# Kernel tuning notes

Measured on AMD Instinct MI355X. Metric: run time of the kernel, lower is better.

## Reference

```python
import jax, jax.numpy as jnp
import numpy as np

B, LQ, LK = 16, 1024, 4096
QD, KD = 512, 512


def setup_inputs() -> dict:
    key = jax.random.key(0)
    ks = jax.random.split(key, 8)
    s = lambda d: 1.0 / np.sqrt(d)
    return {
        "query": jax.random.normal(ks[0], (B, LQ, QD), dtype=jnp.float32),
        "keys": jax.random.normal(ks[1], (B, LK, KD), dtype=jnp.float32),
        "Wq": jax.random.uniform(ks[2], (QD, KD), jnp.float32, -s(QD), s(QD)),
        "bq": jax.random.uniform(ks[3], (KD,), jnp.float32, -s(QD), s(QD)),
        "Wk": jax.random.uniform(ks[4], (KD, KD), jnp.float32, -s(KD), s(KD)),
        "bk": jax.random.uniform(ks[5], (KD,), jnp.float32, -s(KD), s(KD)),
        "Wv": jax.random.uniform(ks[6], (KD, KD), jnp.float32, -s(KD), s(KD)),
        "bv": jax.random.uniform(ks[7], (KD,), jnp.float32, -s(KD), s(KD)),
    }


def reference(query, keys, Wq, bq, Wk, bk, Wv, bv):
    scale = 1.0 / np.sqrt(KD)
    q = query @ Wq + bq                       # [B, LQ, KD]
    k = keys @ Wk + bk                        # [B, LK, KD]
    v = k @ Wv + bv                           # NOTE: value proj applied to projected keys (as in source)
    scores = jnp.einsum('bqd,bkd->bqk', q, k) * scale  # [B, LQ, LK]
    attn = jax.nn.softmax(scores, axis=2)
    context = jnp.einsum('bqk,bkd->bqd', attn, v)      # [B, LQ, KD]
    return context
```

## Files before the change

### kernel.cpp

```cpp
#include <hip/hip_runtime.h>
#include <hip/hip_bf16.h>
#include <stdint.h>


typedef __attribute__((ext_vector_type(8))) short bf16x8;
typedef __attribute__((ext_vector_type(4))) float f32x4;
typedef __attribute__((ext_vector_type(8))) unsigned short ushort8v;
typedef __attribute__((ext_vector_type(4))) unsigned short ushort4v;

__device__ __forceinline__ unsigned short f2bf(float f) {
  union { float f; unsigned int u; } x{f};
  unsigned int r = x.u + 0x7FFFu + ((x.u >> 16) & 1u);
  return (unsigned short)(r >> 16);
}
__device__ __forceinline__ float bf2f(unsigned short h) {
  union { unsigned int u; float f; } x{(unsigned int)h << 16};
  return x.f;
}

#define GLOAD_LDS16(gptr, lptr)                                                  \
  __builtin_amdgcn_global_load_lds((const __attribute__((address_space(1))) void*)(gptr), \
                                   (__attribute__((address_space(3))) void*)(lptr), 16, 0, 0)

__global__ __launch_bounds__(256) void cast_bf16_kernel(const float* __restrict__ in,
                                                        unsigned short* __restrict__ out,
                                                        long n) {
  long i = ((long)blockIdx.x * blockDim.x + threadIdx.x) * 8;
  long stride = (long)gridDim.x * blockDim.x * 8;
  for (; i < n; i += stride) {
    const float4* p = (const float4*)(in + i);
    float4 a = p[0], b = p[1];
    ushort8v o;
    o[0] = f2bf(a.x); o[1] = f2bf(a.y); o[2] = f2bf(a.z); o[3] = f2bf(a.w);
    o[4] = f2bf(b.x); o[5] = f2bf(b.y); o[6] = f2bf(b.z); o[7] = f2bf(b.w);
    *(ushort8v*)(out + i) = o;
  }
}

__global__ __launch_bounds__(256) void transpose_w_kernel(const float* __restrict__ W0,
                                                          const float* __restrict__ W1,
                                                          const float* __restrict__ W2,
                                                          unsigned short* __restrict__ T0,
                                                          unsigned short* __restrict__ T1,
                                                          unsigned short* __restrict__ T2) {
  const float* W = (blockIdx.z == 0) ? W0 : (blockIdx.z == 1) ? W1 : W2;
  unsigned short* T = (blockIdx.z == 0) ? T0 : (blockIdx.z == 1) ? T1 : T2;
  __shared__ float tile[32][33];
  int tx = threadIdx.x & 31, ty = threadIdx.x >> 5;
  int gx = blockIdx.x * 32 + tx;
  int gy0 = blockIdx.y * 32;
#pragma unroll
  for (int i = 0; i < 32; i += 8) tile[ty + i][tx] = W[(size_t)(gy0 + ty + i) * 512 + gx];
  __syncthreads();
  int ox = blockIdx.y * 32 + tx;
  int oy0 = blockIdx.x * 32;
#pragma unroll
  for (int i = 0; i < 32; i += 8)
    T[(size_t)(oy0 + ty + i) * 512 + ox] = f2bf(tile[tx][ty + i]);
}

template <int OUT_MODE>
__global__ __launch_bounds__(256, 2) void gemm_nt(const unsigned short* __restrict__ A,
                                                  const unsigned short* __restrict__ Bt,
                                                  const float* __restrict__ bias,
                                                  void* __restrict__ Cout,
                                                  int M, int N, int K, float scale) {
  __shared__ __align__(16) unsigned short lA[2][128][64];
  __shared__ __align__(16) unsigned short lB[2][128][64];
  const int tid = threadIdx.x;
  const int lane = tid & 63;
  const int wave = tid >> 6;
  const int m0 = blockIdx.y * 128;
  const int n0 = blockIdx.x * 128;

  f32x4 acc[4][4] = {};

  auto stage = [&](int buf, int kt) {
    const int k0 = kt * 64;
#pragma unroll
    for (int p = 0; p < 4; ++p) {
      int c = p * 4 + wave;
      int f = c * 512 + lane * 8;
      int row = f >> 6, col = f & 63;
      const unsigned short* gA = A + (size_t)(m0 + row) * K + (k0 + col);
      const unsigned short* gB = Bt + (size_t)(n0 + row) * K + (k0 + col);
      GLOAD_LDS16(gA, &lA[buf][0][0] + c * 512);
      GLOAD_LDS16(gB, &lB[buf][0][0] + c * 512);
    }
  };

  const int wm = wave >> 1, wn = wave & 1;
  const int lr = lane & 15;
  const int lk = (lane >> 4) << 3;

  const int KT = K >> 6;
  stage(0, 0);
  __syncthreads();
  int cur = 0;
  for (int kt = 0; kt < KT; ++kt) {
    if (kt + 1 < KT) stage(cur ^ 1, kt + 1);
#pragma unroll
    for (int kk = 0; kk < 64; kk += 32) {
      bf16x8 af[4], bfv[4];
#pragma unroll
      for (int i = 0; i < 4; ++i)
        af[i] = *(const bf16x8*)&lA[cur][wm * 64 + i * 16 + lr][kk + lk];
#pragma unroll
      for (int j = 0; j < 4; ++j)
        bfv[j] = *(const bf16x8*)&lB[cur][wn * 64 + j * 16 + lr][kk + lk];
#pragma unroll
      for (int i = 0; i < 4; ++i)
#pragma unroll
        for (int j = 0; j < 4; ++j)
          acc[i][j] = __builtin_amdgcn_mfma_f32_16x16x32_bf16(af[i], bfv[j], acc[i][j], 0, 0, 0);
    }
    __syncthreads();
    cur ^= 1;
  }

  const int ci = lane & 15;
  const int ri = (lane >> 4) * 4;
#pragma unroll
  for (int i = 0; i < 4; ++i) {
#pragma unroll
    for (int j = 0; j < 4; ++j) {
      int gm = m0 + wm * 64 + i * 16 + ri;
      int gn = n0 + wn * 64 + j * 16 + ci;
      float bv_ = bias[gn];
      f32x4 a = acc[i][j];
      if (OUT_MODE == 0) {
        unsigned short* C = (unsigned short*)Cout;
#pragma unroll
        for (int r = 0; r < 4; ++r)
          C[(size_t)(gm + r) * N + gn] = f2bf((a[r] + bv_) * scale);
      } else {
        unsigned short* C = (unsigned short*)Cout;
        int b_ = gm >> 12;
        int ml = gm & 4095;
        ushort4v pk;
#pragma unroll
        for (int r = 0; r < 4; ++r) pk[r] = f2bf((a[r] + bv_) * scale);
        *(ushort4v*)&C[((size_t)b_ * 512 + gn) * 4096 + ml] = pk;
      }
    }
  }
}

__global__ __launch_bounds__(512, 1) void flash_attn(const unsigned short* __restrict__ q,
                                                     const unsigned short* __restrict__ k,
                                                     const unsigned short* __restrict__ vT,
                                                     float* __restrict__ out) {
  __shared__ __align__(16) unsigned short lQ[64 * 512];
  __shared__ __align__(16) unsigned short lK[2][128 * 64];
  __shared__ __align__(16) unsigned short lP[64 * 128];
  __shared__ float redm[64 * 8], reds[64 * 8];
  __shared__ float m_s[64], rs_s[64];

  const int tid = threadIdx.x;
  const int lane = tid & 63;
  const int w = tid >> 6;
  const int bid = blockIdx.x;
  const int b = (bid & 7) * 2 + ((bid >> 3) >> 4);
  const int qt = (bid >> 3) & 15;

  const unsigned short* Qb = q + ((size_t)b * 1024 + qt * 64) * 512;
  const unsigned short* Kb = k + (size_t)b * 4096 * 512;
  const unsigned short* Vb = vT + (size_t)b * 512 * 4096;

  auto stageK = [&](int buf, int t2, int c2) {
    const int kv0 = t2 * 128, kk = c2 * 64;
#pragma unroll
    for (int i = 0; i < 2; ++i) {
      int byte = (i * 512 + tid) * 16;
      int row = byte >> 7;
      int colB = byte & 127;
      int srcB = colB ^ ((row & 7) << 4);
      GLOAD_LDS16(Kb + (size_t)(kv0 + row) * 512 + kk + (srcB >> 1),
                  (char*)&lK[buf][0] + byte);
    }
  };

#pragma unroll
  for (int i = 0; i < 8; ++i) {
    int byte = (i * 512 + tid) * 16;
    int row = byte >> 10;
    int colB = byte & 1023;
    int srcB = (colB & ~127) | ((colB & 127) ^ ((row & 7) << 4));
    GLOAD_LDS16(Qb + (size_t)row * 512 + (srcB >> 1), (char*)lQ + byte);
  }
  stageK(0, 0, 0);
  float m_run = -1e30f, l_run = 0.f;
  float rs_reg = 0.f;
  __syncthreads();

  f32x4 acc_o[4][4] = {};
  int cur = 0;

  for (int t = 0; t < 32; ++t) {
    f32x4 accS[4] = {};
    for (int c = 0; c < 8; ++c) {
      if (c < 7) stageK(cur ^ 1, t, c + 1);
      else if (t < 31) stageK(cur ^ 1, t + 1, 0);
      const int rowK = w * 16 + (lane & 15);
#pragma unroll
      for (int ks = 0; ks < 2; ++ks) {
        int colKB = ((ks * 64 + ((lane >> 4) << 4)) ^ ((rowK & 7) << 4));
        bf16x8 afK = *(const bf16x8*)((char*)&lK[cur][0] + rowK * 128 + colKB);
#pragma unroll
        for (int nf = 0; nf < 4; ++nf) {
          int rowQ = nf * 16 + (lane & 15);
          int colQB = c * 128 + ((ks * 64 + ((lane >> 4) << 4)) ^ ((rowQ & 7) << 4));
          bf16x8 bfQ = *(const bf16x8*)((char*)lQ + rowQ * 1024 + colQB);
          accS[nf] = __builtin_amdgcn_mfma_f32_16x16x32_bf16(afK, bfQ, accS[nf], 0, 0, 0);
        }
      }
      __syncthreads();
      cur ^= 1;
    }

#pragma unroll
    for (int nf = 0; nf < 4; ++nf) {
      f32x4 s = accS[nf];
      float mx = fmaxf(fmaxf(s[0], s[1]), fmaxf(s[2], s[3]));
      mx = fmaxf(mx, __shfl_xor(mx, 16));
      mx = fmaxf(mx, __shfl_xor(mx, 32));
      if (lane < 16) redm[(nf * 16 + lane) * 8 + w] = mx;
    }
    __syncthreads();
    if (w == 0) {
      f32x4 a = *(const f32x4*)&redm[lane * 8];
      f32x4 a2 = *(const f32x4*)&redm[lane * 8 + 4];
      float tmax = fmaxf(fmaxf(fmaxf(a[0], a[1]), fmaxf(a[2], a[3])),
                         fmaxf(fmaxf(a2[0], a2[1]), fmaxf(a2[2], a2[3])));
      float m_new = fmaxf(m_run, tmax);
      rs_reg = __expf(m_run - m_new);
      m_run = m_new;
      m_s[lane] = m_new;
      rs_s[lane] = rs_reg;
    }
    __syncthreads();
#pragma unroll
    for (int nf = 0; nf < 4; ++nf) {
      int qrow = nf * 16 + (lane & 15);
      float mq = m_s[qrow];
      f32x4 s = accS[nf];
      ushort4v pk;
      float sum = 0.f;
#pragma unroll
      for (int r = 0; r < 4; ++r) {
        float p = __expf(s[r] - mq);
        sum += p;
        pk[r] = f2bf(p);
      }
      sum += __shfl_xor(sum, 16);
      sum += __shfl_xor(sum, 32);
      if (lane < 16) reds[qrow * 8 + w] = sum;
      int colB = (w * 32 + ((lane >> 4) << 3)) ^ ((qrow & 7) << 4);
      *(ushort4v*)((char*)lP + qrow * 256 + colB) = pk;
    }
    __syncthreads();
    if (w == 0) {
      f32x4 a = *(const f32x4*)&reds[lane * 8];
      f32x4 a2 = *(const f32x4*)&reds[lane * 8 + 4];
      float tsum = (a[0] + a[1] + a[2] + a[3]) + (a2[0] + a2[1] + a2[2] + a2[3]);
      l_run = l_run * rs_reg + tsum;
    }
#pragma unroll
    for (int mf = 0; mf < 4; ++mf) {
      f32x4 rsv = *(const f32x4*)&rs_s[(mf << 4) + ((lane >> 4) << 2)];
#pragma unroll
      for (int nf = 0; nf < 4; ++nf)
#pragma unroll
        for (int r = 0; r < 4; ++r) acc_o[mf][nf][r] *= rsv[r];
    }
#pragma unroll
    for (int ks = 0; ks < 4; ++ks) {
      bf16x8 bv_[4];
#pragma unroll
      for (int nf = 0; nf < 4; ++nf) {
        int d = (w << 6) + (nf << 4) + (lane & 15);
        bv_[nf] = *(const bf16x8*)(Vb + (size_t)d * 4096 + t * 128 + (ks << 5) + ((lane >> 4) << 3));
      }
#pragma unroll
      for (int mf = 0; mf < 4; ++mf) {
        int qr = (mf << 4) + (lane & 15);
        int colB = ((ks << 6) + ((lane >> 4) << 4)) ^ ((qr & 7) << 4);
        bf16x8 ap = *(const bf16x8*)((char*)lP + qr * 256 + colB);
#pragma unroll
        for (int nf = 0; nf < 4; ++nf)
          acc_o[mf][nf] = __builtin_amdgcn_mfma_f32_16x16x32_bf16(ap, bv_[nf], acc_o[mf][nf], 0, 0, 0);
      }
    }
  }

  if (w == 0) rs_s[lane] = 1.f / l_run;
  __syncthreads();
#pragma unroll
  for (int mf = 0; mf < 4; ++mf) {
    f32x4 il = *(const f32x4*)&rs_s[(mf << 4) + ((lane >> 4) << 2)];
#pragma unroll
    for (int nf = 0; nf < 4; ++nf) {
      int d = (w << 6) + (nf << 4) + (lane & 15);
#pragma unroll
      for (int r = 0; r < 4; ++r) {
        int qr = (mf << 4) + ((lane >> 4) << 2) + r;
        out[((size_t)b * 1024 + qt * 64 + qr) * 512 + d] = acc_o[mf][nf][r] * il[r];
      }
    }
  }
}

extern "C" void kernel_launch(void* const* d_in, const int* in_sizes, int n_in,
                              void* d_out, int out_size, void* d_ws, size_t ws_size,
                              hipStream_t stream) {
  const float* query = (const float*)d_in[0];
  const float* keys  = (const float*)d_in[1];
  const float* Wq = (const float*)d_in[2];
  const float* bq = (const float*)d_in[3];
  const float* Wk = (const float*)d_in[4];
  const float* bk = (const float*)d_in[5];
  const float* Wv = (const float*)d_in[6];
  const float* bv = (const float*)d_in[7];
  float* out = (float*)d_out;

  char* w = (char*)d_ws;
  unsigned short* query_bf = (unsigned short*)w;
  unsigned short* keys_bf  = (unsigned short*)(w + 16777216);
  unsigned short* q_bf = (unsigned short*)(w + 83886080);
  unsigned short* k_bf = (unsigned short*)(w + 100663296);
  unsigned short* vT   = (unsigned short*)(w + 167772160);
  unsigned short* WqT  = (unsigned short*)(w + 234881024);
  unsigned short* WkT  = WqT + 262144;
  unsigned short* WvT  = WkT + 262144;

  const float scale = 0.04419417382415922f;

  cast_bf16_kernel<<<1024, 256, 0, stream>>>(query, query_bf, 8388608L);
  cast_bf16_kernel<<<2048, 256, 0, stream>>>(keys, keys_bf, 33554432L);
  transpose_w_kernel<<<dim3(16, 16, 3), 256, 0, stream>>>(Wq, Wk, Wv, WqT, WkT, WvT);

  gemm_nt<0><<<dim3(4, 128), 256, 0, stream>>>(query_bf, WqT, bq, q_bf,
                                               16384, 512, 512, scale);
  gemm_nt<0><<<dim3(4, 512), 256, 0, stream>>>(keys_bf, WkT, bk, k_bf,
                                               65536, 512, 512, 1.f);
  gemm_nt<1><<<dim3(4, 512), 256, 0, stream>>>(k_bf, WvT, bv, vT,
                                               65536, 512, 512, 1.f);
  flash_attn<<<256, 512, 0, stream>>>(q_bf, k_bf, vT, out);

  (void)in_sizes; (void)n_in; (void)out_size; (void)ws_size;
}
```

Baseline: 702.9 us.

## Load K fragments directly into registers and double-buffer P tile

Drops the LDS-staged, double-buffered K pipeline. Each wave now loads its 16 K rows per 128-key tile straight from global memory into registers, which removes the eight per-chunk barriers in the score loop. V fragments are prefetched into registers before the softmax so their latency overlaps the reductions. P is double-buffered in LDS so the accumulator rescale can move before a barrier. This raises register pressure by 128 extra bf16x8 values. It also gives up shared reuse of K across waves, though each wave reads distinct rows so nothing is duplicated.

Measured after the change: 665.9 us. 5.3% less time.

```diff
diff --git a/kernel.cpp b/kernel.cpp
--- a/kernel.cpp
+++ b/kernel.cpp
@@ -151,14 +151,15 @@
                                                      const unsigned short* __restrict__ vT,
                                                      float* __restrict__ out) {
   __shared__ __align__(16) unsigned short lQ[64 * 512];
-  __shared__ __align__(16) unsigned short lK[2][128 * 64];
-  __shared__ __align__(16) unsigned short lP[64 * 128];
+  __shared__ __align__(16) unsigned short lP[2][64 * 128];
   __shared__ float redm[64 * 8], reds[64 * 8];
   __shared__ float m_s[64], rs_s[64];
 
   const int tid = threadIdx.x;
   const int lane = tid & 63;
   const int w = tid >> 6;
+  const int g = lane >> 4;
+  const int r16 = lane & 15;
   const int bid = blockIdx.x;
   const int b = (bid & 7) * 2 + ((bid >> 3) >> 4);
   const int qt = (bid >> 3) & 15;
@@ -166,19 +167,6 @@
   const unsigned short* Qb = q + ((size_t)b * 1024 + qt * 64) * 512;
   const unsigned short* Kb = k + (size_t)b * 4096 * 512;
   const unsigned short* Vb = vT + (size_t)b * 512 * 4096;
-
-  auto stageK = [&](int buf, int t2, int c2) {
-    const int kv0 = t2 * 128, kk = c2 * 64;
-#pragma unroll
-    for (int i = 0; i < 2; ++i) {
-      int byte = (i * 512 + tid) * 16;
-      int row = byte >> 7;
-      int colB = byte & 127;
-      int srcB = colB ^ ((row & 7) << 4);
-      GLOAD_LDS16(Kb + (size_t)(kv0 + row) * 512 + kk + (srcB >> 1),
-                  (char*)&lK[buf][0] + byte);
-    }
-  };
 
 #pragma unroll
   for (int i = 0; i < 8; ++i) {
@@ -188,34 +176,41 @@
     int srcB = (colB & ~127) | ((colB & 127) ^ ((row & 7) << 4));
     GLOAD_LDS16(Qb + (size_t)row * 512 + (srcB >> 1), (char*)lQ + byte);
   }
-  stageK(0, 0, 0);
   float m_run = -1e30f, l_run = 0.f;
   float rs_reg = 0.f;
   __syncthreads();
 
   f32x4 acc_o[4][4] = {};
-  int cur = 0;
+  const int rowK = w * 16 + r16;
+  const unsigned short* KrowBase = Kb + (size_t)rowK * 512 + (g << 3);
 
   for (int t = 0; t < 32; ++t) {
+    const int pbuf = t & 1;
+    const unsigned short* Krow = KrowBase + (size_t)t * 128 * 512;
+    bf16x8 kf[16];
+#pragma unroll
+    for (int s = 0; s < 16; ++s) kf[s] = *(const bf16x8*)(Krow + s * 32);
+
     f32x4 accS[4] = {};
-    for (int c = 0; c < 8; ++c) {
-      if (c < 7) stageK(cur ^ 1, t, c + 1);
-      else if (t < 31) stageK(cur ^ 1, t + 1, 0);
-      const int rowK = w * 16 + (lane & 15);
-#pragma unroll
-      for (int ks = 0; ks < 2; ++ks) {
-        int colKB = ((ks * 64 + ((lane >> 4) << 4)) ^ ((rowK & 7) << 4));
-        bf16x8 afK = *(const bf16x8*)((char*)&lK[cur][0] + rowK * 128 + colKB);
-#pragma unroll
-        for (int nf = 0; nf < 4; ++nf) {
-          int rowQ = nf * 16 + (lane & 15);
-          int colQB = c * 128 + ((ks * 64 + ((lane >> 4) << 4)) ^ ((rowQ & 7) << 4));
-          bf16x8 bfQ = *(const bf16x8*)((char*)lQ + rowQ * 1024 + colQB);
-          accS[nf] = __builtin_amdgcn_mfma_f32_16x16x32_bf16(afK, bfQ, accS[nf], 0, 0, 0);
-        }
-      }
-      __syncthreads();
-      cur ^= 1;
+#pragma unroll
+    for (int s = 0; s < 16; ++s) {
+#pragma unroll
+      for (int nf = 0; nf < 4; ++nf) {
+        int rowQ = nf * 16 + r16;
+        int base = s * 64 + (g << 4);
+        int colQB = (base & ~127) | ((base & 127) ^ ((rowQ & 7) << 4));
+        bf16x8 qf = *(const bf16x8*)((char*)lQ + rowQ * 1024 + colQB);
+        accS[nf] = __builtin_amdgcn_mfma_f32_16x16x32_bf16(kf[s], qf, accS[nf], 0, 0, 0);
+      }
+    }
+
+    bf16x8 vf[4][4];
+#pragma unroll
+    for (int nf = 0; nf < 4; ++nf) {
+      int d = (w << 6) + (nf << 4) + r16;
+      const unsigned short* Vrow = Vb + (size_t)d * 4096 + t * 128 + (g << 3);
+#pragma unroll
+      for (int ks = 0; ks < 4; ++ks) vf[nf][ks] = *(const bf16x8*)(Vrow + (ks << 5));
     }
 
 #pragma unroll
@@ -241,22 +236,30 @@
     __syncthreads();
 #pragma unroll
     for (int nf = 0; nf < 4; ++nf) {
-      int qrow = nf * 16 + (lane & 15);
+      int qrow = nf * 16 + r16;
       float mq = m_s[qrow];
       f32x4 s = accS[nf];
       ushort4v pk;
       float sum = 0.f;
 #pragma unroll
-      for (int r = 0; r < 4; ++r) {
-        float p = __expf(s[r] - mq);
+      for (int rr = 0; rr < 4; ++rr) {
+        float p = __expf(s[rr] - mq);
         sum += p;
-        pk[r] = f2bf(p);
+        pk[rr] = f2bf(p);
       }
       sum += __shfl_xor(sum, 16);
       sum += __shfl_xor(sum, 32);
       if (lane < 16) reds[qrow * 8 + w] = sum;
-      int colB = (w * 32 + ((lane >> 4) << 3)) ^ ((qrow & 7) << 4);
-      *(ushort4v*)((char*)lP + qrow * 256 + colB) = pk;
+      int colB = (w * 32 + (g << 3)) ^ ((qrow & 7) << 4);
+      *(ushort4v*)((char*)lP[pbuf] + qrow * 256 + colB) = pk;
+    }
+#pragma unroll
+    for (int mf = 0; mf < 4; ++mf) {
+      f32x4 rsv = *(const f32x4*)&rs_s[(mf << 4) + (g << 2)];
+#pragma unroll
+      for (int nf = 0; nf < 4; ++nf)
+#pragma unroll
+        for (int rr = 0; rr < 4; ++rr) acc_o[mf][nf][rr] *= rsv[rr];
     }
     __syncthreads();
     if (w == 0) {
@@ -265,30 +268,17 @@
       float tsum = (a[0] + a[1] + a[2] + a[3]) + (a2[0] + a2[1] + a2[2] + a2[3]);
       l_run = l_run * rs_reg + tsum;
     }
-#pragma unroll
-    for (int mf = 0; mf < 4; ++mf) {
-      f32x4 rsv = *(const f32x4*)&rs_s[(mf << 4) + ((lane >> 4) << 2)];
-#pragma unroll
-      for (int nf = 0; nf < 4; ++nf)
-#pragma unroll
-        for (int r = 0; r < 4; ++r) acc_o[mf][nf][r] *= rsv[r];
-    }
+
 #pragma unroll
     for (int ks = 0; ks < 4; ++ks) {
-      bf16x8 bv_[4];
-#pragma unroll
-      for (int nf = 0; nf < 4; ++nf) {
-        int d = (w << 6) + (nf << 4) + (lane & 15);
-        bv_[nf] = *(const bf16x8*)(Vb + (size_t)d * 4096 + t * 128 + (ks << 5) + ((lane >> 4) << 3));
-      }
 #pragma unroll
       for (int mf = 0; mf < 4; ++mf) {
-        int qr = (mf << 4) + (lane & 15);
-        int colB = ((ks << 6) + ((lane >> 4) << 4)) ^ ((qr & 7) << 4);
-        bf16x8 ap = *(const bf16x8*)((char*)lP + qr * 256 + colB);
+        int qr = (mf << 4) + r16;
+        int colB = ((ks << 6) + (g << 4)) ^ ((qr & 7) << 4);
+        bf16x8 ap = *(const bf16x8*)((char*)lP[pbuf] + qr * 256 + colB);
 #pragma unroll
         for (int nf = 0; nf < 4; ++nf)
-          acc_o[mf][nf] = __builtin_amdgcn_mfma_f32_16x16x32_bf16(ap, bv_[nf], acc_o[mf][nf], 0, 0, 0);
+          acc_o[mf][nf] = __builtin_amdgcn_mfma_f32_16x16x32_bf16(ap, vf[nf][ks], acc_o[mf][nf], 0, 0, 0);
       }
     }
   }
@@ -297,14 +287,14 @@
   __syncthreads();
 #pragma unroll
   for (int mf = 0; mf < 4; ++mf) {
-    f32x4 il = *(const f32x4*)&rs_s[(mf << 4) + ((lane >> 4) << 2)];
+    f32x4 il = *(const f32x4*)&rs_s[(mf << 4) + (g << 2)];
 #pragma unroll
     for (int nf = 0; nf < 4; ++nf) {
-      int d = (w << 6) + (nf << 4) + (lane & 15);
-#pragma unroll
-      for (int r = 0; r < 4; ++r) {
-        int qr = (mf << 4) + ((lane >> 4) << 2) + r;
-        out[((size_t)b * 1024 + qt * 64 + qr) * 512 + d] = acc_o[mf][nf][r] * il[r];
+      int d = (w << 6) + (nf << 4) + r16;
+#pragma unroll
+      for (int rr = 0; rr < 4; ++rr) {
+        int qr = (mf << 4) + (g << 2) + rr;
+        out[((size_t)b * 1024 + qt * 64 + qr) * 512 + d] = acc_o[mf][nf][rr] * il[rr];
       }
     }
   }
```
